# Kernel tuning notes

Hardware: AMD Instinct MI355X
Metric: run time of the kernel (lower is better)

Reference implementation:

```python
import itertools
import jax, jax.numpy as jnp
import numpy as np

# ---- static config (mirrors args) ----
BS = 4; NUM_SEM = 24; C = 4 + NUM_SEM
H_SCREEN = 240; W_SCREEN = 320
FOV = 60.0
RES = 5; Z_RES = 5
MAP_SIZE_CM = 4800 // 2            # global_downscaling = 2
MAP_CELLS = MAP_SIZE_CM // RES     # 480
VR = 100                           # vision_range
AGENT_HEIGHT = 1.55 * 100.0        # cm
MAX_H = int(360 / Z_RES)           # 72
MIN_H = int(-40 / Z_RES)           # -8
MAP_PRED_THR = 1.0; EXP_PRED_THR = 1.0; CAT_PRED_THR = 5.0
SHIFT_X = VR * RES // 2            # 250 cm (shift_loc)
XC = (W_SCREEN - 1.0) / 2.0
ZC = (H_SCREEN - 1.0) / 2.0
FOCAL = (W_SCREEN / 2.0) / float(np.tan(np.deg2rad(FOV / 2.0)))
DEG2RAD = float(np.pi / 180.0)
R2D = 57.29577951308232


def splat_feat_nd(init_grid, feat, coords):
    # init_grid [B,F,D0,D1,D2], feat [B,F,N], coords [B,3,N] in [-1,1]
    B, Fc = init_grid.shape[0], init_grid.shape[1]
    dims = init_grid.shape[2:]
    grid_flat = init_grid.reshape(B, Fc, -1)
    pos_all, wts_all = [], []
    for d in range(len(dims)):
        Dd = dims[d]
        pos = coords[:, d, :] * (Dd / 2.0) + Dd / 2.0   # [B,N]
        fl = jnp.floor(pos)
        pd, wd = [], []
        for off in (0.0, 1.0):
            p = fl + off
            safe = ((p > 0) & (p < Dd)).astype(pos.dtype)
            wd.append((1.0 - jnp.abs(pos - p)) * safe)
            pd.append(p * safe)
        pos_all.append(pd); wts_all.append(wd)
    bidx = jnp.arange(B)[:, None, None]
    fidx = jnp.arange(Fc)[None, :, None]
    for corner in itertools.product((0, 1), repeat=len(dims)):
        index = jnp.zeros_like(pos_all[0][0])
        wts = jnp.ones_like(pos_all[0][0])
        for d in range(len(dims)):
            index = index * dims[d] + pos_all[d][corner[d]]
            wts = wts * wts_all[d][corner[d]]
        idx = index.astype(jnp.int32)[:, None, :]        # [B,1,N]
        grid_flat = grid_flat.at[bidx, fidx, idx].add(feat * wts[:, None, :])
    return jnp.round(grid_flat).reshape(init_grid.shape)


def affine_grid(theta, H, W):
    # align_corners=True base grid; theta [B,2,3] -> grid [B,H,W,2]
    xs = jnp.linspace(-1.0, 1.0, W)
    ys = jnp.linspace(-1.0, 1.0, H)
    gx, gy = jnp.meshgrid(xs, ys)                        # [H,W]
    base = jnp.stack([gx, gy, jnp.ones_like(gx)], axis=-1)
    return jnp.einsum('hwk,bjk->bhwj', base, theta)


def grid_sample(img, grid):
    # bilinear, zero padding, align_corners=True. img [B,C,H,W], grid [B,Ho,Wo,2]
    B, Cc, H, W = img.shape
    ix = (grid[..., 0] + 1.0) * 0.5 * (W - 1)
    iy = (grid[..., 1] + 1.0) * 0.5 * (H - 1)
    x0 = jnp.floor(ix); y0 = jnp.floor(iy)
    x1 = x0 + 1.0; y1 = y0 + 1.0
    wx1 = ix - x0; wx0 = 1.0 - wx1
    wy1 = iy - y0; wy0 = 1.0 - wy1
    bidx = jnp.arange(B)[:, None, None]
    def gather(xi, yi):
        valid = ((xi >= 0) & (xi <= W - 1) & (yi >= 0) & (yi <= H - 1)).astype(img.dtype)
        xc = jnp.clip(xi, 0, W - 1).astype(jnp.int32)
        yc = jnp.clip(yi, 0, H - 1).astype(jnp.int32)
        v = img[bidx, :, yc, xc]                          # [B,Ho,Wo,C]
        return v * valid[..., None]
    out = (gather(x0, y0) * (wx0 * wy0)[..., None]
           + gather(x1, y0) * (wx1 * wy0)[..., None]
           + gather(x0, y1) * (wx0 * wy1)[..., None]
           + gather(x1, y1) * (wx1 * wy1)[..., None])
    return jnp.transpose(out, (0, 3, 1, 2))


def setup_inputs():
    key = jax.random.key(0)
    k1, k2, k3, k4, k5, k6, k7 = jax.random.split(key, 7)
    rgb = jax.random.uniform(k1, (BS, 3, H_SCREEN, W_SCREEN), jnp.float32)
    depth = jax.random.uniform(k2, (BS, 1, H_SCREEN, W_SCREEN), jnp.float32, 50.0, 500.0)  # cm
    seg = jax.random.uniform(k3, (BS, NUM_SEM, H_SCREEN, W_SCREEN), jnp.float32)
    obs = jnp.concatenate([rgb, depth, seg], axis=1)
    pose_obs = jax.random.uniform(k4, (BS, 3), jnp.float32, -0.1, 0.1)
    maps_last = jax.random.uniform(k5, (BS, C, MAP_CELLS, MAP_CELLS), jnp.float32)
    xy = jax.random.uniform(k6, (BS, 2), jnp.float32, 8.0, 16.0)   # meters, inside map
    th = jax.random.uniform(k7, (BS, 1), jnp.float32, -180.0, 180.0)
    poses_last = jnp.concatenate([xy, th], axis=1)
    view_angles = jnp.zeros((BS,), jnp.float32)
    return {"obs": obs, "pose_obs": pose_obs, "maps_last": maps_last,
            "poses_last": poses_last, "view_angles": view_angles, "holding_state": 0}


def _forward(obs, pose_obs, maps_last, poses_last, view_angles):
    bs, c, h, w = obs.shape
    # holding_state == 0 path: mask_err_below = depth < 0
    depth = jnp.where(obs[:, 3] < 0.0, 1e4, obs[:, 3])
    # point cloud from depth (du_scale == 1)
    x_idx = jnp.arange(w, dtype=depth.dtype)
    z_idx = jnp.arange(h - 1, -1, -1).astype(depth.dtype)
    X = (x_idx[None, None, :] - XC) * depth / FOCAL
    Z = (z_idx[None, :, None] - ZC) * depth / FOCAL
    XYZ = jnp.stack([X, depth, Z], axis=-1)              # [bs,h,w,3]
    # camera elevation rotation about x-axis, then add sensor height
    a = view_angles * DEG2RAD
    ca, sa = jnp.cos(a), jnp.sin(a)
    z0 = jnp.zeros_like(ca); o1 = jnp.ones_like(ca)
    Rx = jnp.stack([o1, z0, z0, z0, ca, -sa, z0, sa, ca], -1).reshape(bs, 3, 3)
    XYZ = jnp.einsum('bij,bhwj->bhwi', Rx, XYZ)
    XYZ = XYZ.at[..., 2].add(AGENT_HEIGHT)
    # transform_pose_t with shift_loc: z-rotation by pi/2-pi/2=0, +x shift
    XYZ = XYZ.at[..., 0].add(float(SHIFT_X))
    # normalize to [-1,1] voxel coords
    xy_n = (XYZ[..., :2] / RES - VR // 2.0) / VR * 2.0
    z_n = (XYZ[..., 2] / Z_RES - (MAX_H + MIN_H) // 2.0) / (MAX_H - MIN_H) * 2.0
    coords = jnp.concatenate([xy_n, z_n[..., None]], axis=-1)
    coords = coords.reshape(bs, h * w, 3).transpose(0, 2, 1)            # [bs,3,N]
    feat = jnp.concatenate([jnp.ones((bs, 1, h * w), obs.dtype),
                            obs[:, 4:].reshape(bs, c - 4, h * w)], axis=1)
    init_grid = jnp.zeros((bs, 1 + NUM_SEM, VR, VR, MAX_H - MIN_H), obs.dtype)
    voxels = splat_feat_nd(init_grid, feat, coords).transpose(0, 1, 3, 2, 4)
    min_z = int(15 / Z_RES - MIN_H)
    max_z = int((AGENT_HEIGHT + 1 + 50) / Z_RES - MIN_H)
    agent_height_proj = voxels[..., min_z:max_z].sum(-1)
    all_height_proj = voxels.sum(-1)
    fp_map_pred = jnp.clip(agent_height_proj[:, 0:1] / MAP_PRED_THR, 0.0, 1.0)
    fp_exp_pred = jnp.clip(all_height_proj[:, 0:1] / EXP_PRED_THR, 0.0, 1.0)
    x1 = MAP_CELLS // 2 - VR // 2; x2 = x1 + VR
    y1 = MAP_CELLS // 2; look = VR - 4; y2 = y1 + look
    agent_view = jnp.zeros((bs, c, MAP_CELLS, MAP_CELLS), obs.dtype)
    agent_view = agent_view.at[:, 0:1, y1:y2, x1:x2].set(fp_map_pred[:, :, :look, :])
    agent_view = agent_view.at[:, 1:2, y1:y2, x1:x2].set(fp_exp_pred[:, :, :look, :])
    agent_view = agent_view.at[:, 4:, y1:y2, x1:x2].set(
        jnp.clip(agent_height_proj[:, 1:] / CAT_PRED_THR, 0.0, 1.0)[:, :, :look, :])
    # pose composition (get_new_pose_batch)
    th0 = poses_last[:, 2] / R2D
    ny = poses_last[:, 1] + pose_obs[:, 0] * jnp.sin(th0) + pose_obs[:, 1] * jnp.cos(th0)
    nx = poses_last[:, 0] + pose_obs[:, 0] * jnp.cos(th0) - pose_obs[:, 1] * jnp.sin(th0)
    no = poses_last[:, 2] + pose_obs[:, 2] * R2D
    no = jnp.fmod(no - 180.0, 360.0) + 180.0
    no = jnp.fmod(no + 180.0, 360.0) - 180.0
    current_poses = jnp.stack([nx, ny, no], axis=1)
    st = jax.lax.stop_gradient(current_poses)            # st_pose is .detach()ed
    half = MAP_CELLS // 2
    sx = -(st[:, 0] * 100.0 / RES - half) / half
    sy = -(st[:, 1] * 100.0 / RES - half) / half
    t = (90.0 - st[:, 2]) * DEG2RAD
    ct, s_t = jnp.cos(t), jnp.sin(t)
    zz = jnp.zeros_like(ct); oo = jnp.ones_like(ct)
    theta_rot = jnp.stack([ct, -s_t, zz, s_t, ct, zz], -1).reshape(bs, 2, 3)
    theta_tr = jnp.stack([oo, zz, sx, zz, oo, sy], -1).reshape(bs, 2, 3)
    rot_grid = affine_grid(theta_rot, MAP_CELLS, MAP_CELLS)
    trans_grid = affine_grid(theta_tr, MAP_CELLS, MAP_CELLS)
    rotated = grid_sample(agent_view, rot_grid)
    translated = grid_sample(rotated, trans_grid)
    map_pred = jnp.maximum(maps_last, translated)        # torch.max over stacked pair
    return fp_map_pred, map_pred, current_poses, current_poses


def reference(obs, pose_obs, maps_last, poses_last, view_angles, holding_state):
    # holding_state == 0 path (no object held); branches for 1/2 are host-side numpy.
    return _forward(obs, pose_obs, maps_last, poses_last, view_angles)
```

## Files before the change

### kernel.cpp

```cpp
#include <hip/hip_runtime.h>
#include <math.h>

#define BS 4
#define CC 28
#define NF 25
#define HS 240
#define WSC 320
#define NPIX (HS*WSC)
#define VR 100
#define ZD 80
#define MC 480
#define NCELL (VR*VR)
#define NREC_MAX ((size_t)BS*NPIX*4)
#define NSTRIP 8192
#define ROWS 28

__device__ __forceinline__ float clip01(float v){ return fminf(fmaxf(v, 0.f), 1.f); }

struct Geo {
    float wx[2], wy[2], wz[2];
    int   xi[2], yi[2], zi[2];
    bool  sx[2], sy[2];
};

__device__ __forceinline__ Geo compute_geo(const float* __restrict__ obs,
                                           const float* __restrict__ view_angles,
                                           int b, int pix){
    int j = pix % WSC;
    int i = pix / WSC;
    float depth = obs[((size_t)(b*CC + 3))*NPIX + pix];
    if (depth < 0.f) depth = 10000.f;
    const float FOCAL = 277.12812921102035f;
    float X = ((float)j - 159.5f) * depth / FOCAL;
    float Z = ((float)(HS-1-i) - 119.5f) * depth / FOCAL;
    float a = view_angles[b] * 0.017453292519943295f;
    float ca = cosf(a), sa = sinf(a);
    float Y2 = ca*depth - sa*Z;
    float Z2 = sa*depth + ca*Z + 155.f;
    float X2 = X + 250.f;

    float px = ((X2/5.f - 50.f)/100.f*2.f)*50.f + 50.f;
    float py = ((Y2/5.f - 50.f)/100.f*2.f)*50.f + 50.f;
    float pz = ((Z2/5.f - 32.f)/80.f*2.f)*40.f + 40.f;

    Geo g;
    float fx = floorf(px), fy = floorf(py), fz = floorf(pz);
    {
        float p0 = fx, p1 = fx + 1.f;
        g.sx[0] = (p0 > 0.f) && (p0 < 100.f);
        g.sx[1] = (p1 > 0.f) && (p1 < 100.f);
        g.wx[0] = g.sx[0] ? (1.f - fabsf(px - p0)) : 0.f;
        g.wx[1] = g.sx[1] ? (1.f - fabsf(px - p1)) : 0.f;
        g.xi[0] = g.sx[0] ? (int)p0 : 0;
        g.xi[1] = g.sx[1] ? (int)p1 : 0;
    }
    {
        float p0 = fy, p1 = fy + 1.f;
        g.sy[0] = (p0 > 0.f) && (p0 < 100.f);
        g.sy[1] = (p1 > 0.f) && (p1 < 100.f);
        g.wy[0] = g.sy[0] ? (1.f - fabsf(py - p0)) : 0.f;
        g.wy[1] = g.sy[1] ? (1.f - fabsf(py - p1)) : 0.f;
        g.yi[0] = g.sy[0] ? (int)p0 : 0;
        g.yi[1] = g.sy[1] ? (int)p1 : 0;
    }
    {
        float p0 = fz, p1 = fz + 1.f;
        bool s0 = (p0 > 0.f) && (p0 < 80.f);
        bool s1 = (p1 > 0.f) && (p1 < 80.f);
        g.wz[0] = s0 ? (1.f - fabsf(pz - p0)) : 0.f;
        g.wz[1] = s1 ? (1.f - fabsf(pz - p1)) : 0.f;
        g.zi[0] = s0 ? (int)p0 : 0;
        g.zi[1] = s1 ? (int)p1 : 0;
    }
    return g;
}

__global__ void pose_kernel(const float* __restrict__ pose_obs,
                            const float* __restrict__ poses_last,
                            float* __restrict__ out_p1,
                            float* __restrict__ out_p2,
                            float* __restrict__ params){
    int b = threadIdx.x;
    if (b >= BS) return;
    const float R2D = 57.29577951308232f;
    float th0 = poses_last[b*3+2] / R2D;
    float s0 = sinf(th0), c0 = cosf(th0);
    float ny = poses_last[b*3+1] + pose_obs[b*3+0]*s0 + pose_obs[b*3+1]*c0;
    float nx = poses_last[b*3+0] + pose_obs[b*3+0]*c0 - pose_obs[b*3+1]*s0;
    float no = poses_last[b*3+2] + pose_obs[b*3+2]*R2D;
    no = fmodf(no - 180.f, 360.f) + 180.f;
    no = fmodf(no + 180.f, 360.f) - 180.f;
    out_p1[b*3+0] = nx; out_p1[b*3+1] = ny; out_p1[b*3+2] = no;
    out_p2[b*3+0] = nx; out_p2[b*3+1] = ny; out_p2[b*3+2] = no;
    const float half = 240.f;
    float sx = -(nx*100.f/5.f - half)/half;
    float sy = -(ny*100.f/5.f - half)/half;
    float t = (90.f - no) * 0.017453292519943295f;
    params[b*4+0] = cosf(t);
    params[b*4+1] = sinf(t);
    params[b*4+2] = sx;
    params[b*4+3] = sy;
}

__global__ __launch_bounds__(256)
void prep_kernel(const float* __restrict__ obs,
                 const float* __restrict__ view_angles,
                 int* __restrict__ counts,
                 float* __restrict__ feat){
    __shared__ float sf[6400];
    int t   = threadIdx.x;
    int tid = blockIdx.x * 256 + t;
    int b   = tid / NPIX;
    int pix = tid % NPIX;

    Geo g = compute_geo(obs, view_angles, b, pix);
    #pragma unroll
    for (int cy = 0; cy < 2; ++cy)
    #pragma unroll
    for (int cx = 0; cx < 2; ++cx){
        if (g.sx[cx] && g.sy[cy] && (g.wx[cx]*g.wy[cy] != 0.f))
            atomicAdd(&counts[b*NCELL + g.yi[cy]*VR + g.xi[cx]], 1);
    }

    #pragma unroll 6
    for (int f = 0; f < 24; ++f)
        sf[t*25 + f] = obs[((size_t)(b*CC + 4 + f))*NPIX + pix];
    __syncthreads();
    size_t base = ((size_t)b*NPIX + (size_t)(pix - t)) * 24;
    for (int q = t; q < 6144; q += 256)
        feat[base + q] = sf[q + q/24];
}

__global__ void scan_kernel(const int* __restrict__ counts,
                            int* __restrict__ bases,
                            int* __restrict__ cursor,
                            int* __restrict__ cell_start){
    __shared__ int partC[1024], partW[1024];
    int t = threadIdx.x;
    const int TOT = BS*NCELL;
    const int CH  = 40;
    int beg = t*CH;
    int sc = 0, sw = 0;
    for (int i = 0; i < CH; ++i){
        int idx = beg + i;
        if (idx < TOT){ int c = counts[idx]; sc += c; sw += c + (c ? 24 : 6); }
    }
    partC[t] = sc; partW[t] = sw;
    __syncthreads();
    for (int off = 1; off < 1024; off <<= 1){
        int vc = (t >= off) ? partC[t-off] : 0;
        int vw = (t >= off) ? partW[t-off] : 0;
        __syncthreads();
        partC[t] += vc; partW[t] += vw;
        __syncthreads();
    }
    int totw  = partW[1023];
    int quota = (totw + NSTRIP - 1) / NSTRIP;
    if (quota < 1) quota = 1;
    int runC = (t == 0) ? 0 : partC[t-1];
    int runW = (t == 0) ? 0 : partW[t-1];
    if (t == 0) cell_start[0] = 0;
    for (int i = 0; i < CH; ++i){
        int idx = beg + i;
        if (idx >= TOT) break;
        int c = counts[idx];
        bases[idx]  = runC;
        cursor[idx] = runC;
        int w = c + (c ? 24 : 6);
        int sCur = runW / quota; if (sCur > NSTRIP-1) sCur = NSTRIP-1;
        runC += c; runW += w;
        int sNext = runW / quota; if (sNext > NSTRIP-1) sNext = NSTRIP-1;
        if (idx == TOT-1){
            bases[TOT] = runC;
            for (int gg = sCur+1; gg <= NSTRIP; ++gg) cell_start[gg] = TOT;
        } else {
            for (int gg = sCur+1; gg <= sNext; ++gg) cell_start[gg] = idx+1;
        }
    }
}

__global__ __launch_bounds__(256)
void scatter_kernel(const float* __restrict__ obs,
                    const float* __restrict__ view_angles,
                    int* __restrict__ cursor,
                    uint4* __restrict__ records){
    int tid = blockIdx.x * 256 + threadIdx.x;
    int b   = tid / NPIX;
    int pix = tid % NPIX;
    Geo g = compute_geo(obs, view_angles, b, pix);
    #pragma unroll
    for (int cy = 0; cy < 2; ++cy)
    #pragma unroll
    for (int cx = 0; cx < 2; ++cx){
        float wxy = g.wx[cx] * g.wy[cy];
        if (g.sx[cx] && g.sy[cy] && (wxy != 0.f)){
            int cid = b*NCELL + g.yi[cy]*VR + g.xi[cx];
            int pos = atomicAdd(&cursor[cid], 1);
            float w0 = wxy * g.wz[0];
            float w1 = wxy * g.wz[1];
            unsigned iw = (unsigned)pix | ((unsigned)g.zi[0] << 17)
                                        | ((unsigned)g.zi[1] << 24);
            records[pos] = make_uint4(__float_as_uint(w0), __float_as_uint(w1), iw, 0u);
        }
    }
}

#define GATHER(S, SUB) do{ \
  _Pragma("unroll") \
  for (int u = 0; u < 8; ++u){ \
    int idx = (SUB) + 2*u + rr; \
    bool ok = flane && (idx < n); \
    uint4 rcv = ok ? srec[idx] : Zq; \
    w##S##0[u] = __uint_as_float(rcv.x); \
    w##S##1[u] = __uint_as_float(rcv.y); \
    iw##S[u] = rcv.z; \
    v##S[u] = 1.f; } \
  _Pragma("unroll") \
  for (int u = 0; u < 8; ++u){ \
    int idx = (SUB) + 2*u + rr; \
    if (flane && (idx < n) && f != 0){ \
      int pixq = (int)(iw##S[u] & 0x1FFFFu); \
      v##S[u] = feat_b[(size_t)pixq*24 + (f-1)]; } } \
}while(0)

#define FLUSH(S, SUB) do{ \
  _Pragma("unroll") \
  for (int u = 0; u < 8; ++u){ \
    int idx = (SUB) + 2*u + rr; \
    if (flane && (idx < n)){ \
      unsigned iwv = iw##S[u]; \
      int z0 = (int)((iwv >> 17) & 0x7Fu); \
      int z1 = (int)((iwv >> 24) & 0x7Fu); \
      float w0 = w##S##0[u], w1 = w##S##1[u]; \
      if (w0 != 0.f) atomicAdd(&col[z0*NF + f], v##S[u]*w0); \
      if (w1 != 0.f) atomicAdd(&col[z1*NF + f], v##S[u]*w1); } } \
}while(0)

__global__ __launch_bounds__(64, 4)
void accum_kernel(const uint4* __restrict__ records,
                  const float* __restrict__ feat,
                  const int* __restrict__ bases,
                  const int* __restrict__ cell_start,
                  float* __restrict__ ahp,
                  float* __restrict__ out0){
    __shared__ float col[ZD*NF];
    __shared__ uint4 srec[64];
    __shared__ int   sb[132];

    int g = blockIdx.x;
    int t = threadIdx.x;
    int c0 = cell_start[g];
    int c1 = cell_start[g+1];
    int nc = c1 - c0;
    if (nc <= 0) return;
    int f  = t & 31;
    int rr = t >> 5;
    bool flane = (f < NF);

    for (int i = t; i <= nc; i += 64) sb[i] = bases[c0 + i];
    {   float4* c4 = (float4*)col;
        #pragma unroll
        for (int i = 0; i < 8; ++i){ int idx = t + i*64; if (idx < 500) c4[idx] = make_float4(0,0,0,0); } }

    const uint4 Zq = make_uint4(0u,0u,0u,0u);
    uint4 cur = Zq;
    bool pf = false;

    for (int ci = 0; ci < nc; ++ci){
        int start = sb[ci], end = sb[ci+1];
        int cid = c0 + ci;
        if (start >= end){
            float* row = ahp + (size_t)cid*ROWS;
            if (t < ROWS) row[t] = 0.f;
            if (t == 0)  out0[cid] = 0.f;
            continue;
        }
        int b = cid / NCELL;
        const float* feat_b = feat + (size_t)b*NPIX*24;

        if (!pf){
            int n0 = end - start; if (n0 > 64) n0 = 64;
            cur = (t < n0) ? records[start + t] : Zq;
        }
        pf = false;

        for (int cb = start; cb < end; cb += 64){
            int n = end - cb; if (n > 64) n = 64;
            srec[t] = cur;
            if (cb + 64 < end){
                int n2 = end - cb - 64; if (n2 > 64) n2 = 64;
                cur = (t < n2) ? records[cb + 64 + t] : Zq;
            } else if (ci + 1 < nc){
                int s2 = sb[ci+1], e2 = sb[ci+2];
                if (s2 < e2){
                    int n2 = e2 - s2; if (n2 > 64) n2 = 64;
                    cur = (t < n2) ? records[s2 + t] : Zq;
                    pf = true;
                }
            }
            float wA0[8], wA1[8], vA[8]; unsigned iwA[8];
            float wB0[8], wB1[8], vB[8]; unsigned iwB[8];
            GATHER(A, 0);
            for (int sub = 0; sub < n; ){
                int nx = sub + 16;
                if (nx < n) GATHER(B, nx);
                FLUSH(A, sub);
                sub = nx; if (sub >= n) break;
                nx = sub + 16;
                if (nx < n) GATHER(A, nx);
                FLUSH(B, sub);
                sub = nx;
            }
        }

        {
            int f2 = t % NF, q = t / NF;
            float sall = 0.f, sag = 0.f;
            if (t < 50){
                for (int z = q*40; z < q*40 + 40; ++z){
                    float rv = rintf(col[z*NF + f2]);
                    sall += rv;
                    if (z >= 11 && z < 49) sag += rv;
                }
            }
            float sall_o = __shfl(sall, (t + 25) & 63, 64);
            float sag_o  = __shfl(sag,  (t + 25) & 63, 64);
            float* row = ahp + (size_t)cid*ROWS;
            if (t < NF){
                float a = sag + sag_o;
                float s = sall + sall_o;
                row[t] = a;
                if (t == 0){
                    row[25] = s;
                    out0[cid] = clip01(a);
                }
            } else if (t == 26 || t == 27){
                row[t] = 0.f;
            }
        }
        {   float4* c4 = (float4*)col;
            #pragma unroll
            for (int i = 0; i < 8; ++i){ int idx = t + i*64; if (idx < 500) c4[idx] = make_float4(0,0,0,0); } }
    }
}

__global__ __launch_bounds__(256)
void final_kernel(const float* __restrict__ ahp,
                  const float* __restrict__ params,
                  const float* __restrict__ maps_last,
                  float* __restrict__ out1){
    int tid = blockIdx.x * blockDim.x + threadIdx.x;
    if (tid >= BS*MC*MC) return;
    int w = tid % MC;
    int h = (tid / MC) % MC;
    int b = tid / (MC*MC);

    float ct = params[b*4+0], st = params[b*4+1];
    float sx = params[b*4+2], sy = params[b*4+3];

    float gx = -1.f + 2.f*(float)w/479.f;
    float gy = -1.f + 2.f*(float)h/479.f;
    float ix = (gx + sx + 1.f)*0.5f*479.f;
    float iy = (gy + sy + 1.f)*0.5f*479.f;
    float x0 = floorf(ix), y0 = floorf(iy);
    float wx1 = ix - x0, wx0 = 1.f - wx1;
    float wy1 = iy - y0, wy0 = 1.f - wy1;

    int   offs[16];
    float wt16[16];
    int nz = 0;
    #pragma unroll
    for (int tc = 0; tc < 4; ++tc){
        float txf = (tc & 1) ? x0 + 1.f : x0;
        float tyf = (tc & 2) ? y0 + 1.f : y0;
        float wt  = ((tc & 1) ? wx1 : wx0) * ((tc & 2) ? wy1 : wy0);
        bool validT = (txf >= 0.f) && (txf <= 479.f) && (tyf >= 0.f) && (tyf <= 479.f);
        int txc = (int)fminf(fmaxf(txf, 0.f), 479.f);
        int tyc = (int)fminf(fmaxf(tyf, 0.f), 479.f);

        float gx2 = -1.f + 2.f*(float)txc/479.f;
        float gy2 = -1.f + 2.f*(float)tyc/479.f;
        float rgx = ct*gx2 - st*gy2;
        float rgy = st*gx2 + ct*gy2;
        float ixr = (rgx + 1.f)*0.5f*479.f;
        float iyr = (rgy + 1.f)*0.5f*479.f;
        float rx0 = floorf(ixr), ry0 = floorf(iyr);
        float rwx1 = ixr - rx0, rwx0 = 1.f - rwx1;
        float rwy1 = iyr - ry0, rwy0 = 1.f - rwy1;

        #pragma unroll
        for (int rc = 0; rc < 4; ++rc){
            int id = tc*4 + rc;
            float rxf = (rc & 1) ? rx0 + 1.f : rx0;
            float ryf = (rc & 2) ? ry0 + 1.f : ry0;
            float wr  = ((rc & 1) ? rwx1 : rwx0) * ((rc & 2) ? rwy1 : rwy0);
            bool validR = (rxf >= 0.f) && (rxf <= 479.f) && (ryf >= 0.f) && (ryf <= 479.f);
            int rxc = (int)fminf(fmaxf(rxf, 0.f), 479.f);
            int ryc = (int)fminf(fmaxf(ryf, 0.f), 479.f);
            bool inwin = validT && validR &&
                         (rxc >= 190) && (rxc < 290) && (ryc >= 240) && (ryc < 336);
            float wgt = wt * wr;
            if (inwin && wgt != 0.f){
                offs[id] = (ryc - 240)*VR + (rxc - 190);
                wt16[id] = wgt;
                nz++;
            } else {
                offs[id] = -1;
                wt16[id] = 0.f;
            }
        }
    }

    size_t outBase = (size_t)b*CC*MC*MC + (size_t)h*MC + w;
    if (nz == 0){
        #pragma unroll
        for (int ch = 0; ch < CC; ++ch){
            size_t o = outBase + (size_t)ch*MC*MC;
            out1[o] = fmaxf(maps_last[o], 0.f);
        }
        return;
    }

    const float* ahp_b = ahp + (size_t)b*NCELL*ROWS;
    float acc[26];
    #pragma unroll
    for (int k = 0; k < 26; ++k) acc[k] = 0.f;

    #pragma unroll
    for (int id = 0; id < 16; ++id){
        if (offs[id] < 0) continue;
        float v[28];
        {
            const float4* rp = (const float4*)(ahp_b + (size_t)offs[id]*ROWS);
            #pragma unroll
            for (int k = 0; k < 7; ++k){
                float4 r = rp[k];
                v[4*k]   = r.x; v[4*k+1] = r.y;
                v[4*k+2] = r.z; v[4*k+3] = r.w;
            }
        }
        float wgt = wt16[id];
        acc[0] += wgt * clip01(v[0]);
        acc[1] += wgt * clip01(v[25]);
        #pragma unroll
        for (int ff = 1; ff < 25; ++ff)
            acc[1+ff] += wgt * clip01(v[ff] / 5.f);
    }

    #pragma unroll
    for (int ch = 0; ch < CC; ++ch){
        float a;
        if (ch == 0)      a = acc[0];
        else if (ch == 1) a = acc[1];
        else if (ch < 4)  a = 0.f;
        else              a = acc[ch-2];
        size_t o = outBase + (size_t)ch*MC*MC;
        out1[o] = fmaxf(maps_last[o], a);
    }
}

extern "C" void kernel_launch(void* const* d_in, const int* in_sizes, int n_in,
                              void* d_out, int out_size, void* d_ws, size_t ws_size,
                              hipStream_t stream){
    const float* obs         = (const float*)d_in[0];
    const float* pose_obs    = (const float*)d_in[1];
    const float* maps_last   = (const float*)d_in[2];
    const float* poses_last  = (const float*)d_in[3];
    const float* view_angles = (const float*)d_in[4];
    float* out = (float*)d_out;

    const size_t OUT0 = (size_t)BS*VR*VR;
    const size_t OUT1 = (size_t)BS*CC*MC*MC;
    float* out0 = out;
    float* out1 = out + OUT0;
    float* out2 = out + OUT0 + OUT1;
    float* out3 = out2 + BS*3;

    const size_t AHP_FLOATS  = (size_t)BS*NCELL*ROWS;
    const size_t NCID        = (size_t)BS*NCELL;
    const size_t FEAT_FLOATS = (size_t)BS*NPIX*24;
    const size_t CS_INTS     = NSTRIP + 1;

    float* ahp    = (float*)d_ws;
    float* params = ahp + AHP_FLOATS;
    char*  ws_tail = (char*)(params + 16);
    size_t ws_used_small = (size_t)(ws_tail - (char*)d_ws);

    const size_t BIG_BYTES = (NCID*3 + 1 + CS_INTS)*4 + 64 + NREC_MAX*16 + FEAT_FLOATS*4;
    char* big;
    if (ws_size >= ws_used_small + BIG_BYTES){
        big = ws_tail;
    } else {
        big = (char*)(out1 + OUT1) - BIG_BYTES;
        big = (char*)((uintptr_t)big & ~(uintptr_t)15);
    }
    int* counts     = (int*)big;
    int* bases      = counts + NCID;
    int* cursor     = bases + NCID + 1;
    int* cell_start = cursor + NCID;
    uint4* records = (uint4*)(((uintptr_t)(cell_start + CS_INTS) + 15) & ~(uintptr_t)15);
    float* feat    = (float*)(records + NREC_MAX);

    hipMemsetAsync(counts, 0, NCID*4, stream);
    pose_kernel<<<1, 64, 0, stream>>>(pose_obs, poses_last, out2, out3, params);

    int nblk = (BS*NPIX)/256;
    prep_kernel<<<nblk, 256, 0, stream>>>(obs, view_angles, counts, feat);
    scan_kernel<<<1, 1024, 0, stream>>>(counts, bases, cursor, cell_start);
    scatter_kernel<<<nblk, 256, 0, stream>>>(obs, view_angles, cursor, records);
    accum_kernel<<<NSTRIP, 64, 0, stream>>>(records, feat, bases, cell_start,
                                            ahp, out0);
    final_kernel<<<(BS*MC*MC + 255)/256, 256, 0, stream>>>(ahp, params,
                                                           maps_last, out1);
}
```

Measured before the change: 861.9 us.

## Pad feature rows to 32 floats, slim gather registers, swizzle strip order

```diff
diff --git a/kernel.cpp b/kernel.cpp
--- a/kernel.cpp
+++ b/kernel.cpp
@@ -14,6 +14,8 @@
 #define NREC_MAX ((size_t)BS*NPIX*4)
 #define NSTRIP 8192
 #define ROWS 28
+#define FSTR 32
+#define SBMAX 159
 
 __device__ __forceinline__ float clip01(float v){ return fminf(fmaxf(v, 0.f), 1.f); }
 
@@ -126,9 +128,11 @@
     for (int f = 0; f < 24; ++f)
         sf[t*25 + f] = obs[((size_t)(b*CC + 4 + f))*NPIX + pix];
     __syncthreads();
-    size_t base = ((size_t)b*NPIX + (size_t)(pix - t)) * 24;
-    for (int q = t; q < 6144; q += 256)
-        feat[base + q] = sf[q + q/24];
+    size_t base = ((size_t)b*NPIX + (size_t)(pix - t)) * FSTR;
+    for (int q = t; q < 256*FSTR; q += 256){
+        int pl = q >> 5, ff = q & 31;
+        feat[base + q] = (ff < 24) ? sf[pl*25 + ff] : 0.f;
+    }
 }
 
 __global__ void scan_kernel(const int* __restrict__ counts,
@@ -205,38 +209,29 @@
     }
 }
 
-#define GATHER(S, SUB) do{ \
+
+#define GATHERV(V, SUB) \
   _Pragma("unroll") \
   for (int u = 0; u < 8; ++u){ \
     int idx = (SUB) + 2*u + rr; \
-    bool ok = flane && (idx < n); \
-    uint4 rcv = ok ? srec[idx] : Zq; \
-    w##S##0[u] = __uint_as_float(rcv.x); \
-    w##S##1[u] = __uint_as_float(rcv.y); \
-    iw##S[u] = rcv.z; \
-    v##S[u] = 1.f; } \
+    V[u] = 1.f; \
+    if (flane && idx < n && f != 0){ \
+      int pixq = (int)(srec[idx].z & 0x1FFFFu); \
+      V[u] = feat_b[(size_t)pixq*FSTR + (f-1)]; } }
+
+#define FLUSHV(V, SUB) \
   _Pragma("unroll") \
   for (int u = 0; u < 8; ++u){ \
     int idx = (SUB) + 2*u + rr; \
-    if (flane && (idx < n) && f != 0){ \
-      int pixq = (int)(iw##S[u] & 0x1FFFFu); \
-      v##S[u] = feat_b[(size_t)pixq*24 + (f-1)]; } } \
-}while(0)
-
-#define FLUSH(S, SUB) do{ \
-  _Pragma("unroll") \
-  for (int u = 0; u < 8; ++u){ \
-    int idx = (SUB) + 2*u + rr; \
-    if (flane && (idx < n)){ \
-      unsigned iwv = iw##S[u]; \
-      int z0 = (int)((iwv >> 17) & 0x7Fu); \
-      int z1 = (int)((iwv >> 24) & 0x7Fu); \
-      float w0 = w##S##0[u], w1 = w##S##1[u]; \
-      if (w0 != 0.f) atomicAdd(&col[z0*NF + f], v##S[u]*w0); \
-      if (w1 != 0.f) atomicAdd(&col[z1*NF + f], v##S[u]*w1); } } \
-}while(0)
-
-__global__ __launch_bounds__(64, 4)
+    if (flane && idx < n){ \
+      uint4 rv = srec[idx]; \
+      float w0 = __uint_as_float(rv.x), w1 = __uint_as_float(rv.y); \
+      int z0 = (int)((rv.z >> 17) & 0x7Fu); \
+      int z1 = (int)((rv.z >> 24) & 0x7Fu); \
+      if (w0 != 0.f) atomicAdd(&col[z0*NF + f], V[u]*w0); \
+      if (w1 != 0.f) atomicAdd(&col[z1*NF + f], V[u]*w1); } }
+
+__global__ __launch_bounds__(64)
 void accum_kernel(const uint4* __restrict__ records,
                   const float* __restrict__ feat,
                   const int* __restrict__ bases,
@@ -245,14 +240,16 @@
                   float* __restrict__ out0){
     __shared__ float col[ZD*NF];
     __shared__ uint4 srec[64];
-    __shared__ int   sb[132];
-
-    int g = blockIdx.x;
-    int t = threadIdx.x;
+    __shared__ int   sb[SBMAX+1];
+
+    int g0 = blockIdx.x;
+    int g  = (g0 & 7)*(NSTRIP/8) + (g0 >> 3);
+    int t  = threadIdx.x;
     int c0 = cell_start[g];
     int c1 = cell_start[g+1];
     int nc = c1 - c0;
     if (nc <= 0) return;
+    if (nc > SBMAX) nc = SBMAX;
     int f  = t & 31;
     int rr = t >> 5;
     bool flane = (f < NF);
@@ -276,7 +273,7 @@
             continue;
         }
         int b = cid / NCELL;
-        const float* feat_b = feat + (size_t)b*NPIX*24;
+        const float* feat_b = feat + (size_t)b*NPIX*FSTR;
 
         if (!pf){
             int n0 = end - start; if (n0 > 64) n0 = 64;
@@ -298,17 +295,16 @@
                     pf = true;
                 }
             }
-            float wA0[8], wA1[8], vA[8]; unsigned iwA[8];
-            float wB0[8], wB1[8], vB[8]; unsigned iwB[8];
-            GATHER(A, 0);
+            float vA[8], vB[8];
+            GATHERV(vA, 0);
             for (int sub = 0; sub < n; ){
                 int nx = sub + 16;
-                if (nx < n) GATHER(B, nx);
-                FLUSH(A, sub);
+                if (nx < n) GATHERV(vB, nx);
+                FLUSHV(vA, sub);
                 sub = nx; if (sub >= n) break;
                 nx = sub + 16;
-                if (nx < n) GATHER(A, nx);
-                FLUSH(B, sub);
+                if (nx < n) GATHERV(vA, nx);
+                FLUSHV(vB, sub);
                 sub = nx;
             }
         }
@@ -478,7 +474,7 @@
 
     const size_t AHP_FLOATS  = (size_t)BS*NCELL*ROWS;
     const size_t NCID        = (size_t)BS*NCELL;
-    const size_t FEAT_FLOATS = (size_t)BS*NPIX*24;
+    const size_t FEAT_FLOATS = (size_t)BS*NPIX*FSTR;
     const size_t CS_INTS     = NSTRIP + 1;
 
     float* ahp    = (float*)d_ws;
```

Measured after the change: 866.1 us. About the same (+0.5%).
